# Kernel tuning notes

Measured on AMD Instinct MI355X. Metric: run time of the kernel, lower is better.

## Reference

```python
import jax, jax.numpy as jnp
import numpy as np

B, PRE, NEXT, DIN, DOUT = 256, 64, 32, 128, 64


def _squash(x):
    # x: [..., D]; scale = |x|^2/(1+|x|^2) * x/|x|
    s2 = jnp.sum(x * x, axis=-1, keepdims=True)
    return (s2 / (1.0 + s2)) * x / jnp.sqrt(s2 + 1e-8)


def setup_inputs() -> dict:
    key = jax.random.key(0)
    kx, kw = jax.random.split(key)
    x = jax.random.normal(kx, (B, PRE, DIN), dtype=jnp.float32)
    W = jax.random.normal(kw, (PRE, NEXT, DIN, DOUT), dtype=jnp.float32)
    return {"x": x, "W": W, "iter_time": 3}


def reference(x, W, iter_time):
    Bn = x.shape[0]
    k, K, _, D = W.shape
    # pose predictions: [B, k, K, D]
    p = jnp.einsum('bkd,kKdD->bkKD', x, W)
    b = jnp.zeros((Bn, k, K), dtype=x.dtype)
    q = jnp.zeros((Bn, K, D), dtype=x.dtype)
    for _ in range(iter_time):
        c = jax.nn.softmax(b, axis=-1)                 # [B,k,K]
        q = _squash(jnp.einsum('bkKD,bkK->bKD', p, c))  # [B,K,D]
        b = b + jnp.einsum('bkKD,bKD->bkK', p, q)
    return q.reshape(Bn, -1)
```

## Files before the change

kernel.cpp:

```cpp
#include <hip/hip_runtime.h>
#include <math.h>

#define BATCH 256
#define PRE   64
#define NEXT  32
#define DIN   128
#define DOUT  64

typedef __attribute__((ext_vector_type(8))) short bf16x8;
typedef __attribute__((ext_vector_type(4))) float f32x4;

__device__ __forceinline__ unsigned short f2bf(float f) {
    unsigned u = __float_as_uint(f);
    unsigned r = (u + 0x7fffu + ((u >> 16) & 1u)) >> 16;
    return (unsigned short)r;
}
__device__ __forceinline__ float bf2f(unsigned short h) {
    return __uint_as_float(((unsigned)h) << 16);
}

#define WFRAG_S 10

__global__ __launch_bounds__(256, 2) void gemm_kernel(const float* __restrict__ x,
                                                      const float* __restrict__ W,
                                                      float* __restrict__ p,
                                                      int b0)
{
    __shared__ float xs[128 * 40];
    __shared__ unsigned wpk[256 * WFRAG_S];
    const int K    = blockIdx.x;
    const int kk   = blockIdx.y;
    const int bt   = blockIdx.z;
    const int t    = threadIdx.x;
    const int wave = t >> 6;
    const int lane = t & 63;
    const int ln   = lane & 15;
    const int quad = lane >> 4;
    const int row0 = bt * 128 + wave * 32;

    f32x4 acc[2][4];
#pragma unroll
    for (int mt = 0; mt < 2; ++mt)
#pragma unroll
        for (int nt = 0; nt < 4; ++nt) acc[mt][nt] = (f32x4){0.f, 0.f, 0.f, 0.f};

    const float* Wk = W + (size_t)(kk * NEXT + K) * DIN * DOUT;

    for (int dc = 0; dc < 4; ++dc) {
        __syncthreads();
#pragma unroll
        for (int i = 0; i < 4; ++i) {
            const int f   = t + 256 * i;
            const int row = f >> 3;
            const int d4  = f & 7;
            float4 v = *(const float4*)(x + ((size_t)(b0 + bt * 128 + row) * PRE + kk) * DIN + dc * 32 + d4 * 4);
            *(float4*)&xs[row * 40 + d4 * 4] = v;
        }
#pragma unroll
        for (int it = 0; it < 8; ++it) {
            const int e  = it * 256 + t;
            const int dl = e >> 6;
            const int D  = e & 63;
            float v = Wk[(size_t)(dc * 32 + dl) * DOUT + D];
            unsigned short h = f2bf(v);
            unsigned short l = f2bf(v - bf2f(h));
            const int fr = ((D >> 4) * 64 + (dl >> 3) * 16 + (D & 15));
            wpk[fr * WFRAG_S + (dl & 7)] = (unsigned)h | ((unsigned)l << 16);
        }
        __syncthreads();

        bf16x8 ah[2], al[2];
#pragma unroll
        for (int mt = 0; mt < 2; ++mt) {
            const float* xa = &xs[(wave * 32 + mt * 16 + ln) * 40 + quad * 8];
            float4 v0 = *(const float4*)xa;
            float4 v1 = *(const float4*)(xa + 4);
            float xv[8] = {v0.x, v0.y, v0.z, v0.w, v1.x, v1.y, v1.z, v1.w};
#pragma unroll
            for (int j = 0; j < 8; ++j) {
                unsigned short h = f2bf(xv[j]);
                ah[mt][j] = (short)h;
                al[mt][j] = (short)f2bf(xv[j] - bf2f(h));
            }
        }
        bf16x8 bh[4], bl[4];
#pragma unroll
        for (int nt = 0; nt < 4; ++nt) {
            const unsigned* wp = &wpk[(nt * 64 + quad * 16 + ln) * WFRAG_S];
            unsigned pk[8];
#pragma unroll
            for (int i2 = 0; i2 < 4; ++i2) *(uint2*)&pk[i2 * 2] = *(const uint2*)&wp[i2 * 2];
            union { bf16x8 v; unsigned u[4]; } BH, BL;
#pragma unroll
            for (int i2 = 0; i2 < 4; ++i2) {
                BH.u[i2] = (pk[2 * i2] & 0xffffu) | (pk[2 * i2 + 1] << 16);
                BL.u[i2] = (pk[2 * i2] >> 16) | (pk[2 * i2 + 1] & 0xffff0000u);
            }
            bh[nt] = BH.v; bl[nt] = BL.v;
        }
#pragma unroll
        for (int mt = 0; mt < 2; ++mt)
#pragma unroll
            for (int nt = 0; nt < 4; ++nt) {
                acc[mt][nt] = __builtin_amdgcn_mfma_f32_16x16x32_bf16(ah[mt], bh[nt], acc[mt][nt], 0, 0, 0);
                acc[mt][nt] = __builtin_amdgcn_mfma_f32_16x16x32_bf16(al[mt], bh[nt], acc[mt][nt], 0, 0, 0);
                acc[mt][nt] = __builtin_amdgcn_mfma_f32_16x16x32_bf16(ah[mt], bl[nt], acc[mt][nt], 0, 0, 0);
            }
    }

#pragma unroll
    for (int mt = 0; mt < 2; ++mt)
#pragma unroll
        for (int nt = 0; nt < 4; ++nt) {
            const int D = nt * 16 + ln;
#pragma unroll
            for (int r = 0; r < 4; ++r) {
                const int row = row0 + mt * 16 + quad * 4 + r;
                p[((size_t)(row * PRE + kk) * NEXT + K) * DOUT + D] = acc[mt][nt][r];
            }
        }
}

__global__ __launch_bounds__(512, 1) void route_kernel(const float* __restrict__ p,
                                                       float* __restrict__ out,
                                                       int b0)
{
    __shared__ float qpart[8 * 2048];
    __shared__ float qsum[2048];
    const int b    = blockIdx.x;
    const int t    = threadIdx.x;
    const int w    = t >> 6;
    const int lane = t & 63;
    const int g    = lane >> 4;
    const int m    = lane & 15;
    const float4* pb = (const float4*)(p + (size_t)b * (PRE * NEXT * DOUT));

    for (int idx = t; idx < 2048; idx += 512) qsum[idx] = 0.f;
    __syncthreads();

    for (int pass = 0; pass < 3; ++pass) {
        float4 qa[8];
#pragma unroll
        for (int j = 0; j < 8; ++j) qa[j] = (float4){0.f, 0.f, 0.f, 0.f};

        float4 pv[2][8];
        {
            const size_t sb = (size_t)w * 512;
#pragma unroll
            for (int j = 0; j < 8; ++j) pv[0][j] = pb[sb + j * 64 + lane];
        }
#pragma unroll
        for (int i = 0; i < 8; ++i) {
            const int buf = i & 1;
            if (i < 7) {
                const size_t sb = (size_t)((i + 1) * 8 + w) * 512;
#pragma unroll
                for (int j = 0; j < 8; ++j) pv[buf ^ 1][j] = pb[sb + j * 64 + lane];
            }
            float c[8];
            if (pass == 0) {
#pragma unroll
                for (int j = 0; j < 8; ++j) c[j] = 1.0f / 32.0f;
            } else {
#pragma unroll
                for (int j = 0; j < 8; ++j) {
                    float4 qv = *(const float4*)&qsum[(j * 4 + g) * 64 + m * 4];
                    float d = pv[buf][j].x * qv.x + pv[buf][j].y * qv.y
                            + pv[buf][j].z * qv.z + pv[buf][j].w * qv.w;
                    d += __shfl_xor(d, 1);
                    d += __shfl_xor(d, 2);
                    d += __shfl_xor(d, 4);
                    d += __shfl_xor(d, 8);
                    c[j] = d;
                }
                float mx = c[0];
#pragma unroll
                for (int j = 1; j < 8; ++j) mx = fmaxf(mx, c[j]);
                mx = fmaxf(mx, __shfl_xor(mx, 16));
                mx = fmaxf(mx, __shfl_xor(mx, 32));
                float s = 0.f;
#pragma unroll
                for (int j = 0; j < 8; ++j) { c[j] = __expf(c[j] - mx); s += c[j]; }
                s += __shfl_xor(s, 16);
                s += __shfl_xor(s, 32);
                float inv = 1.0f / s;
#pragma unroll
                for (int j = 0; j < 8; ++j) c[j] *= inv;
            }
#pragma unroll
            for (int j = 0; j < 8; ++j) {
                qa[j].x += c[j] * pv[buf][j].x;
                qa[j].y += c[j] * pv[buf][j].y;
                qa[j].z += c[j] * pv[buf][j].z;
                qa[j].w += c[j] * pv[buf][j].w;
            }
        }
#pragma unroll
        for (int j = 0; j < 8; ++j)
            *(float4*)&qpart[w * 2048 + (j * 4 + g) * 64 + m * 4] = qa[j];
        __syncthreads();

        {
            const int Kq = t >> 4, ch = t & 15;
            float4 v = (float4){0.f, 0.f, 0.f, 0.f};
#pragma unroll
            for (int ww = 0; ww < 8; ++ww) {
                float4 s4 = *(const float4*)&qpart[ww * 2048 + Kq * 64 + ch * 4];
                v.x += s4.x; v.y += s4.y; v.z += s4.z; v.w += s4.w;
            }
            float s2 = v.x * v.x + v.y * v.y + v.z * v.z + v.w * v.w;
            s2 += __shfl_xor(s2, 1);
            s2 += __shfl_xor(s2, 2);
            s2 += __shfl_xor(s2, 4);
            s2 += __shfl_xor(s2, 8);
            float fsc = s2 / ((1.f + s2) * sqrtf(s2 + 1e-8f));
            v.x *= fsc; v.y *= fsc; v.z *= fsc; v.w *= fsc;
            if (pass < 2) {
                float* qd = &qsum[Kq * 64 + ch * 4];
                qd[0] += v.x; qd[1] += v.y; qd[2] += v.z; qd[3] += v.w;
            } else {
                *(float4*)(out + (size_t)(b0 + b) * 2048 + Kq * 64 + ch * 4) = v;
            }
        }
        if (pass < 2) __syncthreads();
    }
}

extern "C" void kernel_launch(void* const* d_in, const int* in_sizes, int n_in,
                              void* d_out, int out_size, void* d_ws, size_t ws_size,
                              hipStream_t stream) {
    const float* x = (const float*)d_in[0];
    const float* W = (const float*)d_in[1];
    float* out = (float*)d_out;
    float* p   = (float*)d_ws;

    const int chunk = (ws_size >= (size_t)134217728) ? 256 : 128;

    for (int b0 = 0; b0 < BATCH; b0 += chunk) {
        gemm_kernel<<<dim3(NEXT, PRE, chunk / 128), 256, 0, stream>>>(x, W, p, b0);
        route_kernel<<<chunk, 512, 0, stream>>>(p, out, b0);
    }
}
```

Before: 272.0 us.

## Reuse converted W tile across batch tiles in GEMM and widen routing blocks

The GEMM kernel no longer launches a z-dimension over batch tiles. Each block now loads and splits its W slice into bf16 hi/lo once, then loops over up to two 128-row batch tiles, so the W global read and conversion are not repeated per batch tile. The cost is a larger x shared buffer and twice the accumulator registers, which can limit occupancy. The routing kernel goes from 512 to 1024 threads, drops the double-buffered prefetch, and adds an extra shared-memory reduction step to combine the partial sums from the 16 waves.

```diff
diff --git a/kernel.cpp b/kernel.cpp
--- a/kernel.cpp
+++ b/kernel.cpp
@@ -21,39 +21,39 @@
 
 #define WFRAG_S 10
 
-__global__ __launch_bounds__(256, 2) void gemm_kernel(const float* __restrict__ x,
+__global__ __launch_bounds__(256, 3) void gemm_kernel(const float* __restrict__ x,
                                                       const float* __restrict__ W,
                                                       float* __restrict__ p,
-                                                      int b0)
+                                                      int b0, int nbt)
 {
-    __shared__ float xs[128 * 40];
+    __shared__ float xs[256 * 40];
     __shared__ unsigned wpk[256 * WFRAG_S];
     const int K    = blockIdx.x;
     const int kk   = blockIdx.y;
-    const int bt   = blockIdx.z;
     const int t    = threadIdx.x;
     const int wave = t >> 6;
     const int lane = t & 63;
     const int ln   = lane & 15;
     const int quad = lane >> 4;
-    const int row0 = bt * 128 + wave * 32;
-
-    f32x4 acc[2][4];
-#pragma unroll
-    for (int mt = 0; mt < 2; ++mt)
-#pragma unroll
-        for (int nt = 0; nt < 4; ++nt) acc[mt][nt] = (f32x4){0.f, 0.f, 0.f, 0.f};
-
-    const float* Wk = W + (size_t)(kk * NEXT + K) * DIN * DOUT;
+
+    f32x4 acc[2][2][4];
+#pragma unroll
+    for (int bt = 0; bt < 2; ++bt)
+#pragma unroll
+        for (int mt = 0; mt < 2; ++mt)
+#pragma unroll
+            for (int nt = 0; nt < 4; ++nt) acc[bt][mt][nt] = (f32x4){0.f, 0.f, 0.f, 0.f};
+
+    const float*  Wk  = W + (size_t)(kk * NEXT + K) * DIN * DOUT;
+    const float4* xg4 = (const float4*)x;
 
     for (int dc = 0; dc < 4; ++dc) {
         __syncthreads();
-#pragma unroll
-        for (int i = 0; i < 4; ++i) {
+        for (int i = 0; i < nbt * 4; ++i) {
             const int f   = t + 256 * i;
             const int row = f >> 3;
             const int d4  = f & 7;
-            float4 v = *(const float4*)(x + ((size_t)(b0 + bt * 128 + row) * PRE + kk) * DIN + dc * 32 + d4 * 4);
+            float4 v = xg4[((size_t)(b0 + row) * PRE + kk) * 32 + dc * 8 + d4];
             *(float4*)&xs[row * 40 + d4 * 4] = v;
         }
 #pragma unroll
@@ -69,20 +69,6 @@
         }
         __syncthreads();
 
-        bf16x8 ah[2], al[2];
-#pragma unroll
-        for (int mt = 0; mt < 2; ++mt) {
-            const float* xa = &xs[(wave * 32 + mt * 16 + ln) * 40 + quad * 8];
-            float4 v0 = *(const float4*)xa;
-            float4 v1 = *(const float4*)(xa + 4);
-            float xv[8] = {v0.x, v0.y, v0.z, v0.w, v1.x, v1.y, v1.z, v1.w};
-#pragma unroll
-            for (int j = 0; j < 8; ++j) {
-                unsigned short h = f2bf(xv[j]);
-                ah[mt][j] = (short)h;
-                al[mt][j] = (short)f2bf(xv[j] - bf2f(h));
-            }
-        }
         bf16x8 bh[4], bl[4];
 #pragma unroll
         for (int nt = 0; nt < 4; ++nt) {
@@ -98,32 +84,50 @@
             }
             bh[nt] = BH.v; bl[nt] = BL.v;
         }
+
+        for (int bt = 0; bt < nbt; ++bt) {
+            bf16x8 ah[2], al[2];
+#pragma unroll
+            for (int mt = 0; mt < 2; ++mt) {
+                const float* xa = &xs[(bt * 128 + wave * 32 + mt * 16 + ln) * 40 + quad * 8];
+                float4 v0 = *(const float4*)xa;
+                float4 v1 = *(const float4*)(xa + 4);
+                float xv[8] = {v0.x, v0.y, v0.z, v0.w, v1.x, v1.y, v1.z, v1.w};
+#pragma unroll
+                for (int j = 0; j < 8; ++j) {
+                    unsigned short h = f2bf(xv[j]);
+                    ah[mt][j] = (short)h;
+                    al[mt][j] = (short)f2bf(xv[j] - bf2f(h));
+                }
+            }
+#pragma unroll
+            for (int mt = 0; mt < 2; ++mt)
+#pragma unroll
+                for (int nt = 0; nt < 4; ++nt) {
+                    acc[bt][mt][nt] = __builtin_amdgcn_mfma_f32_16x16x32_bf16(ah[mt], bh[nt], acc[bt][mt][nt], 0, 0, 0);
+                    acc[bt][mt][nt] = __builtin_amdgcn_mfma_f32_16x16x32_bf16(al[mt], bh[nt], acc[bt][mt][nt], 0, 0, 0);
+                    acc[bt][mt][nt] = __builtin_amdgcn_mfma_f32_16x16x32_bf16(ah[mt], bl[nt], acc[bt][mt][nt], 0, 0, 0);
+                }
+        }
+    }
+
+    for (int bt = 0; bt < nbt; ++bt)
 #pragma unroll
         for (int mt = 0; mt < 2; ++mt)
 #pragma unroll
             for (int nt = 0; nt < 4; ++nt) {
-                acc[mt][nt] = __builtin_amdgcn_mfma_f32_16x16x32_bf16(ah[mt], bh[nt], acc[mt][nt], 0, 0, 0);
-                acc[mt][nt] = __builtin_amdgcn_mfma_f32_16x16x32_bf16(al[mt], bh[nt], acc[mt][nt], 0, 0, 0);
-                acc[mt][nt] = __builtin_amdgcn_mfma_f32_16x16x32_bf16(ah[mt], bl[nt], acc[mt][nt], 0, 0, 0);
-            }
-    }
-
-#pragma unroll
-    for (int mt = 0; mt < 2; ++mt)
-#pragma unroll
-        for (int nt = 0; nt < 4; ++nt) {
-            const int D = nt * 16 + ln;
-#pragma unroll
-            for (int r = 0; r < 4; ++r) {
-                const int row = row0 + mt * 16 + quad * 4 + r;
-                p[((size_t)(row * PRE + kk) * NEXT + K) * DOUT + D] = acc[mt][nt][r];
-            }
-        }
-}
-
-__global__ __launch_bounds__(512, 1) void route_kernel(const float* __restrict__ p,
-                                                       float* __restrict__ out,
-                                                       int b0)
+                const int D = nt * 16 + ln;
+#pragma unroll
+                for (int r = 0; r < 4; ++r) {
+                    const int row = bt * 128 + wave * 32 + mt * 16 + quad * 4 + r;
+                    p[((size_t)(row * PRE + kk) * NEXT + K) * DOUT + D] = acc[bt][mt][nt][r];
+                }
+            }
+}
+
+__global__ __launch_bounds__(1024, 1) void route_kernel(const float* __restrict__ p,
+                                                        float* __restrict__ out,
+                                                        int b0)
 {
     __shared__ float qpart[8 * 2048];
     __shared__ float qsum[2048];
@@ -135,7 +139,7 @@
     const int m    = lane & 15;
     const float4* pb = (const float4*)(p + (size_t)b * (PRE * NEXT * DOUT));
 
-    for (int idx = t; idx < 2048; idx += 512) qsum[idx] = 0.f;
+    for (int idx = t; idx < 2048; idx += 1024) qsum[idx] = 0.f;
     __syncthreads();
 
     for (int pass = 0; pass < 3; ++pass) {
@@ -143,20 +147,13 @@
 #pragma unroll
         for (int j = 0; j < 8; ++j) qa[j] = (float4){0.f, 0.f, 0.f, 0.f};
 
-        float4 pv[2][8];
-        {
-            const size_t sb = (size_t)w * 512;
-#pragma unroll
-            for (int j = 0; j < 8; ++j) pv[0][j] = pb[sb + j * 64 + lane];
-        }
-#pragma unroll
-        for (int i = 0; i < 8; ++i) {
-            const int buf = i & 1;
-            if (i < 7) {
-                const size_t sb = (size_t)((i + 1) * 8 + w) * 512;
-#pragma unroll
-                for (int j = 0; j < 8; ++j) pv[buf ^ 1][j] = pb[sb + j * 64 + lane];
-            }
+#pragma unroll
+        for (int i = 0; i < 4; ++i) {
+            float4 pv[8];
+            const size_t sb = (size_t)(i * 16 + w) * 512;
+#pragma unroll
+            for (int j = 0; j < 8; ++j) pv[j] = pb[sb + j * 64 + lane];
+
             float c[8];
             if (pass == 0) {
 #pragma unroll
@@ -165,8 +162,8 @@
 #pragma unroll
                 for (int j = 0; j < 8; ++j) {
                     float4 qv = *(const float4*)&qsum[(j * 4 + g) * 64 + m * 4];
-                    float d = pv[buf][j].x * qv.x + pv[buf][j].y * qv.y
-                            + pv[buf][j].z * qv.z + pv[buf][j].w * qv.w;
+                    float d = pv[j].x * qv.x + pv[j].y * qv.y
+                            + pv[j].z * qv.z + pv[j].w * qv.w;
                     d += __shfl_xor(d, 1);
                     d += __shfl_xor(d, 2);
                     d += __shfl_xor(d, 4);
@@ -189,18 +186,30 @@
             }
 #pragma unroll
             for (int j = 0; j < 8; ++j) {
-                qa[j].x += c[j] * pv[buf][j].x;
-                qa[j].y += c[j] * pv[buf][j].y;
-                qa[j].z += c[j] * pv[buf][j].z;
-                qa[j].w += c[j] * pv[buf][j].w;
-            }
-        }
-#pragma unroll
-        for (int j = 0; j < 8; ++j)
-            *(float4*)&qpart[w * 2048 + (j * 4 + g) * 64 + m * 4] = qa[j];
-        __syncthreads();
-
-        {
+                qa[j].x += c[j] * pv[j].x;
+                qa[j].y += c[j] * pv[j].y;
+                qa[j].z += c[j] * pv[j].z;
+                qa[j].w += c[j] * pv[j].w;
+            }
+        }
+        if (w < 8) {
+#pragma unroll
+            for (int j = 0; j < 8; ++j)
+                *(float4*)&qpart[w * 2048 + (j * 4 + g) * 64 + m * 4] = qa[j];
+        }
+        __syncthreads();
+        if (w >= 8) {
+#pragma unroll
+            for (int j = 0; j < 8; ++j) {
+                float* dst = &qpart[(w - 8) * 2048 + (j * 4 + g) * 64 + m * 4];
+                float4 cur = *(const float4*)dst;
+                cur.x += qa[j].x; cur.y += qa[j].y; cur.z += qa[j].z; cur.w += qa[j].w;
+                *(float4*)dst = cur;
+            }
+        }
+        __syncthreads();
+
+        if (t < 512) {
             const int Kq = t >> 4, ch = t & 15;
             float4 v = (float4){0.f, 0.f, 0.f, 0.f};
 #pragma unroll
@@ -235,9 +244,10 @@
     float* p   = (float*)d_ws;
 
     const int chunk = (ws_size >= (size_t)134217728) ? 256 : 128;
+    const int nbt   = chunk / 128;
 
     for (int b0 = 0; b0 < BATCH; b0 += chunk) {
-        gemm_kernel<<<dim3(NEXT, PRE, chunk / 128), 256, 0, stream>>>(x, W, p, b0);
-        route_kernel<<<chunk, 512, 0, stream>>>(p, out, b0);
+        gemm_kernel<<<dim3(NEXT, PRE), 256, 0, stream>>>(x, W, p, b0, nbt);
+        route_kernel<<<chunk, 1024, 0, stream>>>(p, out, b0);
     }
 }
```

Measured after the change: 454.3 us. 67.0% more time.

## Reuse packed W fragments across both batch tiles in one GEMM block

Applied to the files above, without the earlier changes.

The GEMM grid drops its batch-tile dimension; each block now loads and splits its W slice into bf16 hi/lo once and applies it to up to two 128-row batch tiles. This removes the duplicated W global reads and conversion work that separate blocks did before. In exchange each block holds twice the accumulators and a larger x shared buffer, which raises register and LDS pressure and halves the grid size. The routing kernel also pads its per-wave partial-sum stride in shared memory, likely to reduce bank conflicts.

```diff
diff --git a/kernel.cpp b/kernel.cpp
--- a/kernel.cpp
+++ b/kernel.cpp
@@ -24,36 +24,36 @@
 __global__ __launch_bounds__(256, 2) void gemm_kernel(const float* __restrict__ x,
                                                       const float* __restrict__ W,
                                                       float* __restrict__ p,
-                                                      int b0)
+                                                      int b0, int nbt)
 {
-    __shared__ float xs[128 * 40];
+    __shared__ float xs[256 * 40];
     __shared__ unsigned wpk[256 * WFRAG_S];
     const int K    = blockIdx.x;
     const int kk   = blockIdx.y;
-    const int bt   = blockIdx.z;
     const int t    = threadIdx.x;
     const int wave = t >> 6;
     const int lane = t & 63;
     const int ln   = lane & 15;
     const int quad = lane >> 4;
-    const int row0 = bt * 128 + wave * 32;
-
-    f32x4 acc[2][4];
-#pragma unroll
-    for (int mt = 0; mt < 2; ++mt)
-#pragma unroll
-        for (int nt = 0; nt < 4; ++nt) acc[mt][nt] = (f32x4){0.f, 0.f, 0.f, 0.f};
-
-    const float* Wk = W + (size_t)(kk * NEXT + K) * DIN * DOUT;
+
+    f32x4 acc[2][2][4];
+#pragma unroll
+    for (int bt = 0; bt < 2; ++bt)
+#pragma unroll
+        for (int mt = 0; mt < 2; ++mt)
+#pragma unroll
+            for (int nt = 0; nt < 4; ++nt) acc[bt][mt][nt] = (f32x4){0.f, 0.f, 0.f, 0.f};
+
+    const float*  Wk  = W + (size_t)(kk * NEXT + K) * DIN * DOUT;
+    const float4* xg4 = (const float4*)x;
 
     for (int dc = 0; dc < 4; ++dc) {
         __syncthreads();
-#pragma unroll
-        for (int i = 0; i < 4; ++i) {
+        for (int i = 0; i < nbt * 4; ++i) {
             const int f   = t + 256 * i;
             const int row = f >> 3;
             const int d4  = f & 7;
-            float4 v = *(const float4*)(x + ((size_t)(b0 + bt * 128 + row) * PRE + kk) * DIN + dc * 32 + d4 * 4);
+            float4 v = xg4[((size_t)(b0 + row) * PRE + kk) * 32 + dc * 8 + d4];
             *(float4*)&xs[row * 40 + d4 * 4] = v;
         }
 #pragma unroll
@@ -69,20 +69,6 @@
         }
         __syncthreads();
 
-        bf16x8 ah[2], al[2];
-#pragma unroll
-        for (int mt = 0; mt < 2; ++mt) {
-            const float* xa = &xs[(wave * 32 + mt * 16 + ln) * 40 + quad * 8];
-            float4 v0 = *(const float4*)xa;
-            float4 v1 = *(const float4*)(xa + 4);
-            float xv[8] = {v0.x, v0.y, v0.z, v0.w, v1.x, v1.y, v1.z, v1.w};
-#pragma unroll
-            for (int j = 0; j < 8; ++j) {
-                unsigned short h = f2bf(xv[j]);
-                ah[mt][j] = (short)h;
-                al[mt][j] = (short)f2bf(xv[j] - bf2f(h));
-            }
-        }
         bf16x8 bh[4], bl[4];
 #pragma unroll
         for (int nt = 0; nt < 4; ++nt) {
@@ -98,34 +84,53 @@
             }
             bh[nt] = BH.v; bl[nt] = BL.v;
         }
+
+        for (int bt = 0; bt < nbt; ++bt) {
+            bf16x8 ah[2], al[2];
+#pragma unroll
+            for (int mt = 0; mt < 2; ++mt) {
+                const float* xa = &xs[(bt * 128 + wave * 32 + mt * 16 + ln) * 40 + quad * 8];
+                float4 v0 = *(const float4*)xa;
+                float4 v1 = *(const float4*)(xa + 4);
+                float xv[8] = {v0.x, v0.y, v0.z, v0.w, v1.x, v1.y, v1.z, v1.w};
+#pragma unroll
+                for (int j = 0; j < 8; ++j) {
+                    unsigned short h = f2bf(xv[j]);
+                    ah[mt][j] = (short)h;
+                    al[mt][j] = (short)f2bf(xv[j] - bf2f(h));
+                }
+            }
+#pragma unroll
+            for (int mt = 0; mt < 2; ++mt)
+#pragma unroll
+                for (int nt = 0; nt < 4; ++nt) {
+                    acc[bt][mt][nt] = __builtin_amdgcn_mfma_f32_16x16x32_bf16(ah[mt], bh[nt], acc[bt][mt][nt], 0, 0, 0);
+                    acc[bt][mt][nt] = __builtin_amdgcn_mfma_f32_16x16x32_bf16(al[mt], bh[nt], acc[bt][mt][nt], 0, 0, 0);
+                    acc[bt][mt][nt] = __builtin_amdgcn_mfma_f32_16x16x32_bf16(ah[mt], bl[nt], acc[bt][mt][nt], 0, 0, 0);
+                }
+        }
+    }
+
+    for (int bt = 0; bt < nbt; ++bt)
 #pragma unroll
         for (int mt = 0; mt < 2; ++mt)
 #pragma unroll
             for (int nt = 0; nt < 4; ++nt) {
-                acc[mt][nt] = __builtin_amdgcn_mfma_f32_16x16x32_bf16(ah[mt], bh[nt], acc[mt][nt], 0, 0, 0);
-                acc[mt][nt] = __builtin_amdgcn_mfma_f32_16x16x32_bf16(al[mt], bh[nt], acc[mt][nt], 0, 0, 0);
-                acc[mt][nt] = __builtin_amdgcn_mfma_f32_16x16x32_bf16(ah[mt], bl[nt], acc[mt][nt], 0, 0, 0);
-            }
-    }
-
-#pragma unroll
-    for (int mt = 0; mt < 2; ++mt)
-#pragma unroll
-        for (int nt = 0; nt < 4; ++nt) {
-            const int D = nt * 16 + ln;
-#pragma unroll
-            for (int r = 0; r < 4; ++r) {
-                const int row = row0 + mt * 16 + quad * 4 + r;
-                p[((size_t)(row * PRE + kk) * NEXT + K) * DOUT + D] = acc[mt][nt][r];
-            }
-        }
-}
-
+                const int D = nt * 16 + ln;
+#pragma unroll
+                for (int r = 0; r < 4; ++r) {
+                    const int row = bt * 128 + wave * 32 + mt * 16 + quad * 4 + r;
+                    p[((size_t)(row * PRE + kk) * NEXT + K) * DOUT + D] = acc[bt][mt][nt][r];
+                }
+            }
+}
+
+#define QP_S 2368
 __global__ __launch_bounds__(512, 1) void route_kernel(const float* __restrict__ p,
                                                        float* __restrict__ out,
                                                        int b0)
 {
-    __shared__ float qpart[8 * 2048];
+    __shared__ float qpart[8 * QP_S];
     __shared__ float qsum[2048];
     const int b    = blockIdx.x;
     const int t    = threadIdx.x;
@@ -197,7 +202,7 @@
         }
 #pragma unroll
         for (int j = 0; j < 8; ++j)
-            *(float4*)&qpart[w * 2048 + (j * 4 + g) * 64 + m * 4] = qa[j];
+            *(float4*)&qpart[w * QP_S + (j * 4 + g) * 64 + m * 4] = qa[j];
         __syncthreads();
 
         {
@@ -205,7 +210,7 @@
             float4 v = (float4){0.f, 0.f, 0.f, 0.f};
 #pragma unroll
             for (int ww = 0; ww < 8; ++ww) {
-                float4 s4 = *(const float4*)&qpart[ww * 2048 + Kq * 64 + ch * 4];
+                float4 s4 = *(const float4*)&qpart[ww * QP_S + Kq * 64 + ch * 4];
                 v.x += s4.x; v.y += s4.y; v.z += s4.z; v.w += s4.w;
             }
             float s2 = v.x * v.x + v.y * v.y + v.z * v.z + v.w * v.w;
@@ -235,9 +240,10 @@
     float* p   = (float*)d_ws;
 
     const int chunk = (ws_size >= (size_t)134217728) ? 256 : 128;
+    const int nbt   = chunk / 128;
 
     for (int b0 = 0; b0 < BATCH; b0 += chunk) {
-        gemm_kernel<<<dim3(NEXT, PRE, chunk / 128), 256, 0, stream>>>(x, W, p, b0);
+        gemm_kernel<<<dim3(NEXT, PRE), 256, 0, stream>>>(x, W, p, b0, nbt);
         route_kernel<<<chunk, 512, 0, stream>>>(p, out, b0);
     }
 }
```

Result: slower. 474.9 us (+74.6%).
